# Kernel optimization log

Measured on AMD Instinct MI355X. Metric: run time of the kernel, lower is better.

The kernel has to match this reference:

```python
import jax, jax.numpy as jnp
import numpy as np

NUM_IN, NUM_OUT, SD, BATCH = 2048, 8192, 5, 4096
INIT_DELTA = 0.01


def _dist(a, b):
    # a: [I,1,D], b: [1,O,D] -> [I,O]
    return jnp.sqrt(jnp.sum((a - b) ** 2, axis=-1))


def setup_inputs() -> dict:
    key = jax.random.key(0)
    k1, k2, k3, k4, k5 = jax.random.split(key, 5)
    init_in_pos = jax.random.normal(k1, (NUM_IN, 1, SD), dtype=jnp.float32)
    init_out_pos = jax.random.normal(k2, (1, NUM_OUT, SD), dtype=jnp.float32)
    in_pos = init_in_pos + INIT_DELTA * jax.random.normal(k3, (NUM_IN, 1, SD), dtype=jnp.float32)
    out_pos = init_out_pos + INIT_DELTA * jax.random.normal(k4, (1, NUM_OUT, SD), dtype=jnp.float32)
    inputs = jax.random.normal(k5, (BATCH, NUM_IN), dtype=jnp.float32)
    biases = jnp.zeros((NUM_OUT,), dtype=jnp.float32)
    return {"inputs": inputs, "init_in_pos": init_in_pos, "init_out_pos": init_out_pos,
            "in_pos": in_pos, "out_pos": out_pos, "biases": biases}


def reference(inputs, init_in_pos, init_out_pos, in_pos, out_pos, biases):
    # weight = ||in_pos - out_pos|| - ||init_in_pos - init_out_pos||, shape [I,O]
    w = _dist(in_pos, out_pos) - _dist(init_in_pos, init_out_pos)
    return inputs @ w + biases
```

## Files before the change

kernel.cpp:

```cpp
#include <hip/hip_runtime.h>
#include <hip/hip_bf16.h>
#include <stdint.h>

#define NUM_IN  2048
#define NUM_OUT 8192
#define BATCH   4096
#define SD      5

#define BM 256
#define BN 256
#define BK 32
#define NT (NUM_IN / BK)
#define TILEE (BM * BK)

typedef __bf16 bf16x8 __attribute__((ext_vector_type(8)));
typedef float  f32x4  __attribute__((ext_vector_type(4)));
typedef unsigned short ushort_t;
typedef ushort_t ushort8 __attribute__((ext_vector_type(8)));

static __device__ __forceinline__ ushort_t bf16_bits(float f) {
  __hip_bfloat16 h = __float2bfloat16(f);
  ushort_t u;
  __builtin_memcpy(&u, &h, 2);
  return u;
}

__global__ __launch_bounds__(256) void cvt_kernel(const float* __restrict__ x,
                                                  ushort_t* __restrict__ y) {
  const int i = (blockIdx.x * 256 + threadIdx.x) * 8;
  float4 v0 = *reinterpret_cast<const float4*>(x + i);
  float4 v1 = *reinterpret_cast<const float4*>(x + i + 4);
  ushort8 o;
  o[0] = bf16_bits(v0.x); o[1] = bf16_bits(v0.y);
  o[2] = bf16_bits(v0.z); o[3] = bf16_bits(v0.w);
  o[4] = bf16_bits(v1.x); o[5] = bf16_bits(v1.y);
  o[6] = bf16_bits(v1.z); o[7] = bf16_bits(v1.w);
  *reinterpret_cast<ushort8*>(y + i) = o;
}

__global__ __launch_bounds__(256) void genw_kernel(
    const float* __restrict__ in_pos, const float* __restrict__ out_pos,
    const float* __restrict__ init_in, const float* __restrict__ init_out,
    ushort_t* __restrict__ Wt) {
  __shared__ float s_ip[NUM_IN * SD];
  __shared__ float s_iip[NUM_IN * SD];
  const int tid = threadIdx.x;
#pragma unroll
  for (int i = 0; i < 10; ++i) {
    const int idx = i * 1024 + tid * 4;
    *reinterpret_cast<float4*>(&s_ip[idx]) =
        *reinterpret_cast<const float4*>(in_pos + idx);
    *reinterpret_cast<float4*>(&s_iip[idx]) =
        *reinterpret_cast<const float4*>(init_in + idx);
  }
  __syncthreads();

  const int n  = blockIdx.x * 16 + (tid >> 4);
  const int kg = tid & 15;
  float op[SD], iop[SD];
#pragma unroll
  for (int d = 0; d < SD; ++d) {
    op[d]  = out_pos[n * SD + d];
    iop[d] = init_out[n * SD + d];
  }
#pragma unroll 1
  for (int kb = 0; kb < 16; ++kb) {
    const int k0 = kb * 128 + kg * 8;
    float buf[40], ibuf[40];
#pragma unroll
    for (int j = 0; j < 10; ++j) {
      float4 v = *reinterpret_cast<const float4*>(&s_ip[k0 * SD + j * 4]);
      buf[4 * j + 0] = v.x; buf[4 * j + 1] = v.y;
      buf[4 * j + 2] = v.z; buf[4 * j + 3] = v.w;
      float4 u = *reinterpret_cast<const float4*>(&s_iip[k0 * SD + j * 4]);
      ibuf[4 * j + 0] = u.x; ibuf[4 * j + 1] = u.y;
      ibuf[4 * j + 2] = u.z; ibuf[4 * j + 3] = u.w;
    }
    ushort8 o;
#pragma unroll
    for (int i = 0; i < 8; ++i) {
      float d1 = 0.f, d0 = 0.f;
#pragma unroll
      for (int d = 0; d < SD; ++d) {
        float a = buf[i * SD + d] - op[d];
        float b = ibuf[i * SD + d] - iop[d];
        d1 += a * a;
        d0 += b * b;
      }
      o[i] = bf16_bits(sqrtf(d1) - sqrtf(d0));
    }
    *reinterpret_cast<ushort8*>(Wt + (size_t)n * NUM_IN + k0) = o;
  }
}

__global__ __launch_bounds__(512, 1) void gemm_kernel(
    const ushort_t* __restrict__ A,
    const ushort_t* __restrict__ Bt,
    const float* __restrict__ bias,
    float* __restrict__ C) {
  __shared__ __align__(16) ushort_t sA[2 * TILEE];
  __shared__ __align__(16) ushort_t sB[2 * TILEE];

  const int tid  = threadIdx.x;
  const int w    = tid >> 6;
  const int l    = tid & 63;
  const int wm   = w >> 2;
  const int wn   = w & 3;
  const int lrow = l & 15;
  const int lkc  = l >> 4;

  const int orig = blockIdx.x;
  const int lin  = (orig & 7) * 64 + (orig >> 3);
  const int bx   = lin >> 4;
  const int by   = lin & 15;
  const int m0   = by * BM;
  const int n0   = bx * BN;

  const int phys  = ((4 * (lrow & 1) + lkc) ^ (lrow >> 1));
  const int laneo = (lrow >> 1) * 64 + phys * 8;
  const int AbW = wm * 4096;
  const int BbW = wn * 2048;

  const int cc  = (tid & 7) ^ ((tid >> 3) & 7);
  const int row = 2 * (tid >> 3) + (cc >> 2);
  const int ke  = (cc & 3) * 8;
  const ushort_t* pA0 = A  + (size_t)(m0 + row) * NUM_IN + ke;
  const ushort_t* pA1 = A  + (size_t)(m0 + row + 128) * NUM_IN + ke;
  const ushort_t* pB0 = Bt + (size_t)(n0 + row) * NUM_IN + ke;
  const ushort_t* pB1 = Bt + (size_t)(n0 + row + 128) * NUM_IN + ke;

#define GLDS(src, dst)                                                         \
  __builtin_amdgcn_global_load_lds(                                            \
      reinterpret_cast<const __attribute__((address_space(1))) uint32_t*>(     \
          (uintptr_t)(src)),                                                   \
      reinterpret_cast<__attribute__((address_space(3))) uint32_t*>(           \
          (uintptr_t)(dst)),                                                   \
      16, 0, 0)

#define STAGE(bs, kt)                                                          \
  {                                                                            \
    GLDS(pA0 + (kt), &sA[(bs) * TILEE + tid * 8]);                             \
    GLDS(pA1 + (kt), &sA[(bs) * TILEE + tid * 8 + 4096]);                      \
    GLDS(pB0 + (kt), &sB[(bs) * TILEE + tid * 8]);                             \
    GLDS(pB1 + (kt), &sB[(bs) * TILEE + tid * 8 + 4096]);                      \
  }

#define RD_A(arr, bs, mh)                                                      \
  {                                                                            \
    _Pragma("unroll")                                                          \
    for (int mi = 0; mi < 4; ++mi)                                             \
      arr[mi] = *reinterpret_cast<const bf16x8*>(                              \
          &sA[(bs) * TILEE + AbW + (mh) * 2048 + mi * 512 + laneo]);           \
  }
#define RD_B(arr, bs, nh)                                                      \
  {                                                                            \
    _Pragma("unroll")                                                          \
    for (int nj = 0; nj < 2; ++nj)                                             \
      arr[nj] = *reinterpret_cast<const bf16x8*>(                              \
          &sB[(bs) * TILEE + BbW + (nh) * 1024 + nj * 512 + laneo]);           \
  }

#define MFMA8(mh, nh, Aa, Bx)                                                  \
  {                                                                            \
    __builtin_amdgcn_s_setprio(1);                                             \
    _Pragma("unroll")                                                          \
    for (int mi = 0; mi < 4; ++mi)                                             \
      _Pragma("unroll")                                                        \
      for (int nj = 0; nj < 2; ++nj)                                           \
        acc[(mh) * 4 + mi][(nh) * 2 + nj] =                                    \
            __builtin_amdgcn_mfma_f32_16x16x32_bf16(                           \
                Aa[mi], Bx[nj], acc[(mh) * 4 + mi][(nh) * 2 + nj], 0, 0, 0);   \
    __builtin_amdgcn_s_setprio(0);                                             \
  }

#define LGKM(n)  asm volatile("s_waitcnt lgkmcnt(" #n ")" ::: "memory")
#define SCHED0   __builtin_amdgcn_sched_barrier(0)
#define BARRIER  __builtin_amdgcn_s_barrier()
#define VMCNT0   asm volatile("s_waitcnt vmcnt(0)" ::: "memory")

#define KTILE(CUR, NXT, ktn)                                                   \
  {                                                                            \
    STAGE(NXT, ktn)                                                            \
    RD_A(aE, CUR, 0) RD_B(b0, CUR, 0)                                          \
    RD_B(b1, CUR, 1)                                                           \
    LGKM(2); SCHED0;                                                           \
    MFMA8(0, 0, aE, b0)                                                        \
    RD_A(aO, CUR, 1)                                                           \
    LGKM(4); SCHED0;                                                           \
    MFMA8(0, 1, aE, b1)                                                        \
    LGKM(0); SCHED0;                                                           \
    MFMA8(1, 0, aO, b0)                                                        \
    MFMA8(1, 1, aO, b1)                                                        \
    VMCNT0;                                                                    \
    BARRIER;                                                                   \
  }

  f32x4 acc[8][4];
#pragma unroll
  for (int i = 0; i < 8; ++i)
#pragma unroll
    for (int j = 0; j < 4; ++j) acc[i][j] = f32x4{0.f, 0.f, 0.f, 0.f};

  bf16x8 aE[4], aO[4], b0[2], b1[2];

  STAGE(0, 0)
  VMCNT0;
  BARRIER;

#pragma unroll 1
  for (int tt = 0; tt < NT; tt += 2) {
    const int k1 = (tt + 1 < NT ? tt + 1 : NT - 1) * BK;
    const int k2 = (tt + 2 < NT ? tt + 2 : NT - 1) * BK;
    KTILE(0, 1, k1)
    KTILE(1, 0, k2)
  }

  const int er = l >> 4;
  const int ec = l & 15;
#pragma unroll
  for (int nh = 0; nh < 2; ++nh) {
#pragma unroll
    for (int nj = 0; nj < 2; ++nj) {
      const int col = n0 + wn * 64 + nh * 32 + nj * 16 + ec;
      const float bi = bias[col];
#pragma unroll
      for (int mh = 0; mh < 2; ++mh) {
#pragma unroll
        for (int mi = 0; mi < 4; ++mi) {
#pragma unroll
          for (int j = 0; j < 4; ++j) {
            const int row = m0 + wm * 128 + mh * 64 + mi * 16 + er * 4 + j;
            C[(size_t)row * NUM_OUT + col] =
                acc[mh * 4 + mi][nh * 2 + nj][j] + bi;
          }
        }
      }
    }
  }
#undef KTILE
#undef STAGE
#undef RD_A
#undef RD_B
#undef MFMA8
#undef GLDS
}

extern "C" void kernel_launch(void* const* d_in, const int* in_sizes, int n_in,
                              void* d_out, int out_size, void* d_ws, size_t ws_size,
                              hipStream_t stream) {
  const float* inputs   = (const float*)d_in[0];
  const float* init_in  = (const float*)d_in[1];
  const float* init_out = (const float*)d_in[2];
  const float* in_pos   = (const float*)d_in[3];
  const float* out_pos  = (const float*)d_in[4];
  const float* biases   = (const float*)d_in[5];
  float* out = (float*)d_out;

  ushort_t* Abf = (ushort_t*)d_ws;
  ushort_t* Wt  = (ushort_t*)((char*)d_ws + (size_t)BATCH * NUM_IN * 2);

  cvt_kernel<<<(BATCH * NUM_IN) / (256 * 8), 256, 0, stream>>>(inputs, Abf);
  genw_kernel<<<NUM_OUT / 16, 256, 0, stream>>>(
      in_pos, out_pos, init_in, init_out, Wt);
  gemm_kernel<<<(BATCH / BM) * (NUM_OUT / BN), 512, 0, stream>>>(
      Abf, Wt, biases, out);
}
```

Baseline: 175.0 us.

## Shrink GEMM block tile to 256x128 with four waves per block

Halves the N dimension of the GEMM block tile and drops from eight waves to four per block (2x2 wave grid), doubling the number of blocks. The global-to-LDS staging is reworked so each thread issues four A loads and two B loads per k-tile, and the block-index swizzle is adjusted for the larger grid. The aim is to reduce LDS footprint and improve occupancy or tail balance across CUs. The cost is lower arithmetic intensity per block and more redundant A-tile traffic.

```diff
diff --git a/kernel.cpp b/kernel.cpp
--- a/kernel.cpp
+++ b/kernel.cpp
@@ -8,10 +8,11 @@
 #define SD      5
 
 #define BM 256
-#define BN 256
+#define BN 128
 #define BK 32
 #define NT (NUM_IN / BK)
-#define TILEE (BM * BK)
+#define ATILEE (BM * BK)
+#define BTILEE (BN * BK)
 
 typedef __bf16 bf16x8 __attribute__((ext_vector_type(8)));
 typedef float  f32x4  __attribute__((ext_vector_type(4)));
@@ -93,24 +94,24 @@
   }
 }
 
-__global__ __launch_bounds__(512, 1) void gemm_kernel(
+__global__ __launch_bounds__(256, 1) void gemm_kernel(
     const ushort_t* __restrict__ A,
     const ushort_t* __restrict__ Bt,
     const float* __restrict__ bias,
     float* __restrict__ C) {
-  __shared__ __align__(16) ushort_t sA[2 * TILEE];
-  __shared__ __align__(16) ushort_t sB[2 * TILEE];
+  __shared__ __align__(16) ushort_t sA[2 * ATILEE];
+  __shared__ __align__(16) ushort_t sB[2 * BTILEE];
 
   const int tid  = threadIdx.x;
   const int w    = tid >> 6;
   const int l    = tid & 63;
-  const int wm   = w >> 2;
-  const int wn   = w & 3;
+  const int wm   = w >> 1;
+  const int wn   = w & 1;
   const int lrow = l & 15;
   const int lkc  = l >> 4;
 
   const int orig = blockIdx.x;
-  const int lin  = (orig & 7) * 64 + (orig >> 3);
+  const int lin  = (orig & 7) * 128 + (orig >> 3);
   const int bx   = lin >> 4;
   const int by   = lin & 15;
   const int m0   = by * BM;
@@ -121,13 +122,26 @@
   const int AbW = wm * 4096;
   const int BbW = wn * 2048;
 
-  const int cc  = (tid & 7) ^ ((tid >> 3) & 7);
-  const int row = 2 * (tid >> 3) + (cc >> 2);
-  const int ke  = (cc & 3) * 8;
-  const ushort_t* pA0 = A  + (size_t)(m0 + row) * NUM_IN + ke;
-  const ushort_t* pA1 = A  + (size_t)(m0 + row + 128) * NUM_IN + ke;
-  const ushort_t* pB0 = Bt + (size_t)(n0 + row) * NUM_IN + ke;
-  const ushort_t* pB1 = Bt + (size_t)(n0 + row + 128) * NUM_IN + ke;
+#define SRC_GEOM(d, rowv, kev)                                                 \
+  {                                                                            \
+    const int c_ = ((d) & 7) ^ (((d) >> 3) & 7);                               \
+    rowv = 2 * ((d) >> 3) + (c_ >> 2);                                         \
+    kev  = (c_ & 3) * 8;                                                       \
+  }
+  int rA0, kA0, rA1, kA1, rA2, kA2e, rA3, kA3;
+  int rB0, kB0, rB1, kB1;
+  SRC_GEOM(tid,        rA0, kA0)
+  SRC_GEOM(tid + 256,  rA1, kA1)
+  SRC_GEOM(tid + 512,  rA2, kA2e)
+  SRC_GEOM(tid + 768,  rA3, kA3)
+  rB0 = rA0; kB0 = kA0;
+  rB1 = rA1; kB1 = kA1;
+  const ushort_t* pA0 = A  + (size_t)(m0 + rA0) * NUM_IN + kA0;
+  const ushort_t* pA1 = A  + (size_t)(m0 + rA1) * NUM_IN + kA1;
+  const ushort_t* pA2 = A  + (size_t)(m0 + rA2) * NUM_IN + kA2e;
+  const ushort_t* pA3 = A  + (size_t)(m0 + rA3) * NUM_IN + kA3;
+  const ushort_t* pB0 = Bt + (size_t)(n0 + rB0) * NUM_IN + kB0;
+  const ushort_t* pB1 = Bt + (size_t)(n0 + rB1) * NUM_IN + kB1;
 
 #define GLDS(src, dst)                                                         \
   __builtin_amdgcn_global_load_lds(                                            \
@@ -139,10 +153,12 @@
 
 #define STAGE(bs, kt)                                                          \
   {                                                                            \
-    GLDS(pA0 + (kt), &sA[(bs) * TILEE + tid * 8]);                             \
-    GLDS(pA1 + (kt), &sA[(bs) * TILEE + tid * 8 + 4096]);                      \
-    GLDS(pB0 + (kt), &sB[(bs) * TILEE + tid * 8]);                             \
-    GLDS(pB1 + (kt), &sB[(bs) * TILEE + tid * 8 + 4096]);                      \
+    GLDS(pA0 + (kt), &sA[(bs) * ATILEE + tid * 8]);                            \
+    GLDS(pA1 + (kt), &sA[(bs) * ATILEE + tid * 8 + 2048]);                     \
+    GLDS(pA2 + (kt), &sA[(bs) * ATILEE + tid * 8 + 4096]);                     \
+    GLDS(pA3 + (kt), &sA[(bs) * ATILEE + tid * 8 + 6144]);                     \
+    GLDS(pB0 + (kt), &sB[(bs) * BTILEE + tid * 8]);                            \
+    GLDS(pB1 + (kt), &sB[(bs) * BTILEE + tid * 8 + 2048]);                     \
   }
 
 #define RD_A(arr, bs, mh)                                                      \
@@ -150,14 +166,14 @@
     _Pragma("unroll")                                                          \
     for (int mi = 0; mi < 4; ++mi)                                             \
       arr[mi] = *reinterpret_cast<const bf16x8*>(                              \
-          &sA[(bs) * TILEE + AbW + (mh) * 2048 + mi * 512 + laneo]);           \
+          &sA[(bs) * ATILEE + AbW + (mh) * 2048 + mi * 512 + laneo]);          \
   }
 #define RD_B(arr, bs, nh)                                                      \
   {                                                                            \
     _Pragma("unroll")                                                          \
     for (int nj = 0; nj < 2; ++nj)                                             \
       arr[nj] = *reinterpret_cast<const bf16x8*>(                              \
-          &sB[(bs) * TILEE + BbW + (nh) * 1024 + nj * 512 + laneo]);           \
+          &sB[(bs) * BTILEE + BbW + (nh) * 1024 + nj * 512 + laneo]);          \
   }
 
 #define MFMA8(mh, nh, Aa, Bx)                                                  \
@@ -243,6 +259,7 @@
 #undef RD_B
 #undef MFMA8
 #undef GLDS
+#undef SRC_GEOM
 }
 
 extern "C" void kernel_launch(void* const* d_in, const int* in_sizes, int n_in,
@@ -262,6 +279,6 @@
   cvt_kernel<<<(BATCH * NUM_IN) / (256 * 8), 256, 0, stream>>>(inputs, Abf);
   genw_kernel<<<NUM_OUT / 16, 256, 0, stream>>>(
       in_pos, out_pos, init_in, init_out, Wt);
-  gemm_kernel<<<(BATCH / BM) * (NUM_OUT / BN), 512, 0, stream>>>(
+  gemm_kernel<<<(BATCH / BM) * (NUM_OUT / BN), 256, 0, stream>>>(
       Abf, Wt, biases, out);
 }
```

Result: slower. 283.9 us (+62.2%).
